# Performance work log

Hardware: AMD Instinct MI355X
Metric: run time of the kernel (lower is better)

Reference implementation:

```python
import jax, jax.numpy as jnp
import numpy as np

B, S, H = 2, 2048, 1024
E, I, K = 8, 4096, 2


def setup_inputs() -> dict:
    key = jax.random.key(0)
    ks = jax.random.split(key, 5)
    scale_h = 1.0 / np.sqrt(H)
    scale_i = 1.0 / np.sqrt(I)
    x = jax.random.normal(ks[0], (B, S, H), dtype=jnp.float32)
    gate_w = jax.random.normal(ks[1], (E, H), dtype=jnp.float32) * scale_h   # router Linear weight [out=E, in=H]
    wg = jax.random.normal(ks[2], (E, I, H), dtype=jnp.float32) * scale_h    # gate_proj weights, stacked over experts
    wu = jax.random.normal(ks[3], (E, I, H), dtype=jnp.float32) * scale_h    # up_proj weights
    wd = jax.random.normal(ks[4], (E, H, I), dtype=jnp.float32) * scale_i    # down_proj weights
    return {"x": x, "gate_w": gate_w, "wg": wg, "wu": wu, "wd": wd}


def _moe_forward(x, gate_w, wg, wu, wd):
    b, s, h = x.shape
    x_flat = x.reshape(-1, h)                       # [T, H]
    logits = x_flat @ gate_w.T                      # [T, E]
    top_v, top_i = jax.lax.top_k(logits, K)         # [T, K]
    probs = jax.nn.softmax(top_v.astype(jnp.float32), axis=-1).astype(logits.dtype)  # [T, K]
    # per-token combine weight for each expert: sum_k probs[:,k] * 1[top_i[:,k]==e]
    one_hot = jax.nn.one_hot(top_i, E, dtype=probs.dtype)   # [T, K, E]
    combine = jnp.einsum('tk,tke->et', probs, one_hot)       # [E, T]
    # loop over experts via scan: acc += w_e * SwiGLU_e(x)
    def body(acc, ws):
        wge, wue, wde, we = ws
        hidden = jax.nn.silu(x_flat @ wge.T) * (x_flat @ wue.T)  # [T, I]
        return acc + we[:, None] * (hidden @ wde.T), None
    out, _ = jax.lax.scan(body, jnp.zeros_like(x_flat), (wg, wu, wd, combine))
    return out.reshape(b, s, h)


def reference(x, gate_w, wg, wu, wd):
    return _moe_forward(x, gate_w, wg, wu, wd)
```

## Files before the change

kernel.cpp:

```cpp
#include <hip/hip_runtime.h>
#include <math.h>

#define T_TOK 4096
#define H_DIM 1024
#define E_NUM 8
#define I_DIM 4096
#define KSPLIT 4

typedef __attribute__((ext_vector_type(4))) float f32x4;
typedef __attribute__((ext_vector_type(8))) short bf16x8;

__device__ inline unsigned short f2bf(float f) {
  unsigned int u = __float_as_uint(f);
  u += 0x7fffu + ((u >> 16) & 1u);
  return (unsigned short)(u >> 16);
}

__device__ inline void cvt_store4(unsigned short* dst, const float* src) {
  f32x4 v = *reinterpret_cast<const f32x4*>(src);
  ushort4 o;
  o.x = f2bf(v[0]); o.y = f2bf(v[1]); o.z = f2bf(v[2]); o.w = f2bf(v[3]);
  *reinterpret_cast<ushort4*>(dst) = o;
}

__device__ inline void gll16(const void* g, void* l) {
  __builtin_amdgcn_global_load_lds(
      (const __attribute__((address_space(1))) void*)g,
      (__attribute__((address_space(3))) void*)l, 16, 0, 0);
}

__global__ __launch_bounds__(64) void k_router(const float* __restrict__ x,
                                               const float* __restrict__ gw,
                                               unsigned short* __restrict__ xb,
                                               int2* __restrict__ tokE,
                                               float2* __restrict__ tokP,
                                               int* __restrict__ counts) {
  const int t = blockIdx.x;
  const int l = threadIdx.x;
  const float* xr = x + (size_t)t * H_DIM;
  unsigned short* xbr = xb ? xb + (size_t)t * H_DIM : nullptr;
  float acc[E_NUM];
#pragma unroll
  for (int e = 0; e < E_NUM; e++) acc[e] = 0.f;
  for (int h = l; h < H_DIM; h += 64) {
    float xv = xr[h];
    if (xbr) xbr[h] = f2bf(xv);
#pragma unroll
    for (int e = 0; e < E_NUM; e++) acc[e] += xv * gw[e * H_DIM + h];
  }
#pragma unroll
  for (int e = 0; e < E_NUM; e++) {
#pragma unroll
    for (int off = 32; off > 0; off >>= 1) acc[e] += __shfl_xor(acc[e], off);
  }
  if (l == 0) {
    float v0 = -1e30f, v1 = -1e30f;
    int e0 = 0, e1 = 0;
#pragma unroll
    for (int e = 0; e < E_NUM; e++) {
      float v = acc[e];
      if (v > v0) { v1 = v0; e1 = e0; v0 = v; e0 = e; }
      else if (v > v1) { v1 = v; e1 = e; }
    }
    float ex = expf(v1 - v0);
    float p0 = 1.f / (1.f + ex);
    float p1 = ex * p0;
    tokE[t] = make_int2(e0, e1);
    tokP[t] = make_float2(p0, p1);
    atomicAdd(&counts[e0], 1);
    atomicAdd(&counts[e1], 1);
  }
}

__global__ void k_offsets(const int* __restrict__ counts, int* __restrict__ offsets) {
  if (threadIdx.x == 0 && blockIdx.x == 0) {
    int s = 0;
    for (int e = 0; e < E_NUM; e++) { offsets[e] = s; s += counts[e]; }
    offsets[E_NUM] = s;
  }
}

__global__ __launch_bounds__(256) void k_scatter(const int2* __restrict__ tokE,
                                                 const float2* __restrict__ tokP,
                                                 const int* __restrict__ offsets,
                                                 int* __restrict__ cursor,
                                                 int* __restrict__ slot_tok,
                                                 float* __restrict__ slot_w) {
  int t = blockIdx.x * 256 + threadIdx.x;
  if (t >= T_TOK) return;
  int2 e = tokE[t];
  float2 p = tokP[t];
  int pos0 = atomicAdd(&cursor[e.x], 1);
  slot_tok[offsets[e.x] + pos0] = t;
  slot_w[offsets[e.x] + pos0] = p.x;
  int pos1 = atomicAdd(&cursor[e.y], 1);
  slot_tok[offsets[e.y] + pos1] = t;
  slot_w[offsets[e.y] + pos1] = p.y;
}

__global__ __launch_bounds__(256) void k_cvt(const float* __restrict__ src,
                                             unsigned short* __restrict__ dst,
                                             int n4) {
  int i = blockIdx.x * 256 + threadIdx.x;
  const int stride = gridDim.x * 256;
  for (; i < n4; i += stride) {
    f32x4 v = reinterpret_cast<const f32x4*>(src)[i];
    ushort4 o;
    o.x = f2bf(v[0]); o.y = f2bf(v[1]); o.z = f2bf(v[2]); o.w = f2bf(v[3]);
    reinterpret_cast<ushort4*>(dst)[i] = o;
  }
}

__global__ __launch_bounds__(256, 2) void k_gateup2(
    const unsigned short* __restrict__ xb, const unsigned short* __restrict__ wgb,
    const unsigned short* __restrict__ wub, const int* __restrict__ counts,
    const int* __restrict__ offsets, const int* __restrict__ slot_tok,
    unsigned short* __restrict__ hidden) {
  const int e = blockIdx.z;
  const int cnt = counts[e];
  const int m0 = blockIdx.y * 128;
  if (m0 >= cnt) return;
  const int n0 = blockIdx.x * 128;
  const int base = offsets[e];

  __shared__ unsigned short As[128 * 64];
  __shared__ unsigned short Bg[128 * 64];
  __shared__ unsigned short Bu[128 * 64];

  const int tid = threadIdx.x;
  const int wave = tid >> 6;
  const int lane = tid & 63;
  const int wm = (wave >> 1) * 64;
  const int wn = (wave & 1) * 64;
  const int lr = lane & 15;
  const int lk = lane >> 4;

  const int sr = lane >> 3;
  const int sc = lane & 7;
  const int swz = ((sc ^ sr) << 3);

  const size_t wbase = (size_t)e * I_DIM * H_DIM;
  const unsigned short* srcA[4];
  const unsigned short* srcBg[4];
  const unsigned short* srcBu[4];
  unsigned short* dstA[4];
  unsigned short* dstBg[4];
  unsigned short* dstBu[4];
#pragma unroll
  for (int i = 0; i < 4; i++) {
    int row = wave * 32 + i * 8 + sr;
    int gr = m0 + row; if (gr > cnt - 1) gr = cnt - 1;
    srcA[i]  = xb + (size_t)slot_tok[base + gr] * H_DIM + swz;
    srcBg[i] = wgb + wbase + (size_t)(n0 + row) * H_DIM + swz;
    srcBu[i] = wub + wbase + (size_t)(n0 + row) * H_DIM + swz;
    dstA[i]  = &As[(wave * 32 + i * 8) * 64];
    dstBg[i] = &Bg[(wave * 32 + i * 8) * 64];
    dstBu[i] = &Bu[(wave * 32 + i * 8) * 64];
  }

  f32x4 accg[4][4], accu[4][4];
#pragma unroll
  for (int i = 0; i < 4; i++)
#pragma unroll
    for (int j = 0; j < 4; j++) {
      accg[i][j] = (f32x4){0.f, 0.f, 0.f, 0.f};
      accu[i][j] = (f32x4){0.f, 0.f, 0.f, 0.f};
    }

  const int xorr = ((lr & 7) << 3);

  for (int k0 = 0; k0 < H_DIM; k0 += 64) {
#pragma unroll
    for (int i = 0; i < 4; i++) {
      gll16(srcA[i] + k0, dstA[i]);
      gll16(srcBg[i] + k0, dstBg[i]);
      gll16(srcBu[i] + k0, dstBu[i]);
    }
    __syncthreads();
#pragma unroll
    for (int kh = 0; kh < 2; kh++) {
      const int koff = (((kh * 4 + lk) << 3) ^ xorr);
      bf16x8 af[4];
#pragma unroll
      for (int mf = 0; mf < 4; mf++)
        af[mf] = *reinterpret_cast<const bf16x8*>(&As[(wm + mf * 16 + lr) * 64 + koff]);
#pragma unroll
      for (int nf = 0; nf < 4; nf++) {
        const int roff = (wn + nf * 16 + lr) * 64 + koff;
        bf16x8 bg = *reinterpret_cast<const bf16x8*>(&Bg[roff]);
        bf16x8 bu = *reinterpret_cast<const bf16x8*>(&Bu[roff]);
#pragma unroll
        for (int mf = 0; mf < 4; mf++) {
          accg[mf][nf] = __builtin_amdgcn_mfma_f32_16x16x32_bf16(af[mf], bg, accg[mf][nf], 0, 0, 0);
          accu[mf][nf] = __builtin_amdgcn_mfma_f32_16x16x32_bf16(af[mf], bu, accu[mf][nf], 0, 0, 0);
        }
      }
    }
    __syncthreads();
  }

#pragma unroll
  for (int mf = 0; mf < 4; mf++) {
#pragma unroll
    for (int j = 0; j < 4; j++) {
      int row = wm + mf * 16 + lk * 4 + j;
      if (m0 + row < cnt) {
        size_t hbase = (size_t)(base + m0 + row) * I_DIM;
#pragma unroll
        for (int nf = 0; nf < 4; nf++) {
          int col = n0 + wn + nf * 16 + lr;
          float g = accg[mf][nf][j];
          float u = accu[mf][nf][j];
          float h = g / (1.f + expf(-g)) * u;
          hidden[hbase + col] = f2bf(h);
        }
      }
    }
  }
}

__global__ __launch_bounds__(256, 2) void k_down6(
    const unsigned short* __restrict__ hidden, const unsigned short* __restrict__ wdb,
    const int* __restrict__ counts, const int* __restrict__ offsets,
    const int* __restrict__ slot_tok, const float* __restrict__ slot_w,
    float* __restrict__ out) {
  const int zz = blockIdx.z;
  const int e = zz >> 2;
  const int ks = zz & 3;
  const int cnt = counts[e];
  const int m0 = blockIdx.y * 128;
  if (m0 >= cnt) return;
  const int n0 = blockIdx.x * 128;
  const int base = offsets[e];
  const int kbeg = ks * (I_DIM / KSPLIT);
  const int kend = kbeg + I_DIM / KSPLIT;

  __shared__ unsigned short As[128 * 64];
  __shared__ unsigned short Bs[128 * 64];

  const int tid = threadIdx.x;
  const int wave = tid >> 6;
  const int lane = tid & 63;
  const int wm = (wave >> 1) * 64;
  const int wn = (wave & 1) * 64;
  const int lr = lane & 15;
  const int lk = lane >> 4;

  const int sr = lane >> 3;
  const int sc = lane & 7;
  const int swz = ((sc ^ sr) << 3);

  const unsigned short* srcA[4];
  const unsigned short* srcB[4];
  unsigned short* dstA[4];
  unsigned short* dstB[4];
#pragma unroll
  for (int i = 0; i < 4; i++) {
    int row = wave * 32 + i * 8 + sr;
    int gr = m0 + row; if (gr > cnt - 1) gr = cnt - 1;
    srcA[i] = hidden + (size_t)(base + gr) * I_DIM + swz;
    srcB[i] = wdb + (size_t)e * H_DIM * I_DIM + (size_t)(n0 + row) * I_DIM + swz;
    dstA[i] = &As[(wave * 32 + i * 8) * 64];
    dstB[i] = &Bs[(wave * 32 + i * 8) * 64];
  }

  f32x4 acc[4][4];
#pragma unroll
  for (int i = 0; i < 4; i++)
#pragma unroll
    for (int j = 0; j < 4; j++) acc[i][j] = (f32x4){0.f, 0.f, 0.f, 0.f};

  const int xorr = ((lr & 7) << 3);

  for (int k0 = kbeg; k0 < kend; k0 += 64) {
#pragma unroll
    for (int i = 0; i < 4; i++) {
      gll16(srcA[i] + k0, dstA[i]);
      gll16(srcB[i] + k0, dstB[i]);
    }
    __syncthreads();
#pragma unroll
    for (int kh = 0; kh < 2; kh++) {
      const int koff = (((kh * 4 + lk) << 3) ^ xorr);
      bf16x8 af[4];
#pragma unroll
      for (int mf = 0; mf < 4; mf++)
        af[mf] = *reinterpret_cast<const bf16x8*>(&As[(wm + mf * 16 + lr) * 64 + koff]);
#pragma unroll
      for (int nf = 0; nf < 4; nf++) {
        bf16x8 bf = *reinterpret_cast<const bf16x8*>(&Bs[(wn + nf * 16 + lr) * 64 + koff]);
#pragma unroll
        for (int mf = 0; mf < 4; mf++)
          acc[mf][nf] = __builtin_amdgcn_mfma_f32_16x16x32_bf16(af[mf], bf, acc[mf][nf], 0, 0, 0);
      }
    }
    __syncthreads();
  }

#pragma unroll
  for (int mf = 0; mf < 4; mf++) {
#pragma unroll
    for (int j = 0; j < 4; j++) {
      int row = wm + mf * 16 + lk * 4 + j;
      if (m0 + row < cnt) {
        int slot = base + m0 + row;
        int t = slot_tok[slot];
        float w = slot_w[slot];
#pragma unroll
        for (int nf = 0; nf < 4; nf++) {
          int col = n0 + wn + nf * 16 + lr;
          atomicAdd(&out[(size_t)t * H_DIM + col], w * acc[mf][nf][j]);
        }
      }
    }
  }
}

__global__ __launch_bounds__(256) void k_gateup_v1(
    const float* __restrict__ x, const float* __restrict__ wg,
    const float* __restrict__ wu, const int* __restrict__ counts,
    const int* __restrict__ offsets, const int* __restrict__ slot_tok,
    unsigned short* __restrict__ hidden) {
  const int e = blockIdx.z;
  const int cnt = counts[e];
  const int m0 = blockIdx.y * 128;
  if (m0 >= cnt) return;
  const int n0 = blockIdx.x * 128;
  const int base = offsets[e];

  __shared__ unsigned short As[128 * 40];
  __shared__ unsigned short Bgs[128 * 40];
  __shared__ unsigned short Bus[128 * 40];

  const int tid = threadIdx.x;
  const int wave = tid >> 6;
  const int lane = tid & 63;
  const int wm = (wave >> 1) * 64;
  const int wn = (wave & 1) * 64;
  const int lr = lane & 15;
  const int lk = lane >> 4;
  const int r_sub = tid >> 3;
  const int kq = (tid & 7) * 4;

  const float* wge = wg + (size_t)e * I_DIM * H_DIM;
  const float* wue = wu + (size_t)e * I_DIM * H_DIM;

  const float* aptr[4];
  const float* bgptr[4];
  const float* buptr[4];
#pragma unroll
  for (int p = 0; p < 4; p++) {
    int row = p * 32 + r_sub;
    int gr = m0 + row;
    if (gr > cnt - 1) gr = cnt - 1;
    aptr[p] = x + (size_t)slot_tok[base + gr] * H_DIM + kq;
    bgptr[p] = wge + (size_t)(n0 + row) * H_DIM + kq;
    buptr[p] = wue + (size_t)(n0 + row) * H_DIM + kq;
  }

  f32x4 accg[4][4], accu[4][4];
#pragma unroll
  for (int i = 0; i < 4; i++)
#pragma unroll
    for (int j = 0; j < 4; j++) {
      accg[i][j] = (f32x4){0.f, 0.f, 0.f, 0.f};
      accu[i][j] = (f32x4){0.f, 0.f, 0.f, 0.f};
    }

  for (int k0 = 0; k0 < H_DIM; k0 += 32) {
#pragma unroll
    for (int p = 0; p < 4; p++) {
      int row = p * 32 + r_sub;
      cvt_store4(&As[row * 40 + kq], aptr[p] + k0);
      cvt_store4(&Bgs[row * 40 + kq], bgptr[p] + k0);
      cvt_store4(&Bus[row * 40 + kq], buptr[p] + k0);
    }
    __syncthreads();
    bf16x8 af[4];
#pragma unroll
    for (int mf = 0; mf < 4; mf++)
      af[mf] = *reinterpret_cast<const bf16x8*>(&As[(wm + mf * 16 + lr) * 40 + lk * 8]);
#pragma unroll
    for (int nf = 0; nf < 4; nf++) {
      bf16x8 bg = *reinterpret_cast<const bf16x8*>(&Bgs[(wn + nf * 16 + lr) * 40 + lk * 8]);
      bf16x8 bu = *reinterpret_cast<const bf16x8*>(&Bus[(wn + nf * 16 + lr) * 40 + lk * 8]);
#pragma unroll
      for (int mf = 0; mf < 4; mf++) {
        accg[mf][nf] = __builtin_amdgcn_mfma_f32_16x16x32_bf16(af[mf], bg, accg[mf][nf], 0, 0, 0);
        accu[mf][nf] = __builtin_amdgcn_mfma_f32_16x16x32_bf16(af[mf], bu, accu[mf][nf], 0, 0, 0);
      }
    }
    __syncthreads();
  }

#pragma unroll
  for (int mf = 0; mf < 4; mf++) {
#pragma unroll
    for (int j = 0; j < 4; j++) {
      int row = wm + mf * 16 + lk * 4 + j;
      if (m0 + row < cnt) {
        size_t hbase = (size_t)(base + m0 + row) * I_DIM;
#pragma unroll
        for (int nf = 0; nf < 4; nf++) {
          int col = n0 + wn + nf * 16 + lr;
          float g = accg[mf][nf][j];
          float u = accu[mf][nf][j];
          float h = g / (1.f + expf(-g)) * u;
          hidden[hbase + col] = f2bf(h);
        }
      }
    }
  }
}

__global__ __launch_bounds__(256) void k_down_v1(
    const unsigned short* __restrict__ hidden, const float* __restrict__ wd,
    const int* __restrict__ counts, const int* __restrict__ offsets,
    const int* __restrict__ slot_tok, const float* __restrict__ slot_w,
    float* __restrict__ out) {
  const int e = blockIdx.z;
  const int cnt = counts[e];
  const int m0 = blockIdx.y * 128;
  if (m0 >= cnt) return;
  const int n0 = blockIdx.x * 128;
  const int base = offsets[e];

  __shared__ unsigned short As[128 * 40];
  __shared__ unsigned short Bs[128 * 40];

  const int tid = threadIdx.x;
  const int wave = tid >> 6;
  const int lane = tid & 63;
  const int wm = (wave >> 1) * 64;
  const int wn = (wave & 1) * 64;
  const int lr = lane & 15;
  const int lk = lane >> 4;
  const int r_sub = tid >> 3;
  const int kq = (tid & 7) * 4;

  const unsigned short* ap[4];
  const float* bp[4];
#pragma unroll
  for (int p = 0; p < 4; p++) {
    int row = p * 32 + r_sub;
    int gr = m0 + row;
    if (gr > cnt - 1) gr = cnt - 1;
    ap[p] = hidden + (size_t)(base + gr) * I_DIM + kq;
    bp[p] = wd + (size_t)e * H_DIM * I_DIM + (size_t)(n0 + row) * I_DIM + kq;
  }

  f32x4 acc[4][4];
#pragma unroll
  for (int i = 0; i < 4; i++)
#pragma unroll
    for (int j = 0; j < 4; j++) acc[i][j] = (f32x4){0.f, 0.f, 0.f, 0.f};

  for (int k0 = 0; k0 < I_DIM; k0 += 32) {
#pragma unroll
    for (int p = 0; p < 4; p++) {
      int row = p * 32 + r_sub;
      *reinterpret_cast<ushort4*>(&As[row * 40 + kq]) =
          *reinterpret_cast<const ushort4*>(ap[p] + k0);
      cvt_store4(&Bs[row * 40 + kq], bp[p] + k0);
    }
    __syncthreads();
    bf16x8 af[4];
#pragma unroll
    for (int mf = 0; mf < 4; mf++)
      af[mf] = *reinterpret_cast<const bf16x8*>(&As[(wm + mf * 16 + lr) * 40 + lk * 8]);
#pragma unroll
    for (int nf = 0; nf < 4; nf++) {
      bf16x8 bf = *reinterpret_cast<const bf16x8*>(&Bs[(wn + nf * 16 + lr) * 40 + lk * 8]);
#pragma unroll
      for (int mf = 0; mf < 4; mf++)
        acc[mf][nf] = __builtin_amdgcn_mfma_f32_16x16x32_bf16(af[mf], bf, acc[mf][nf], 0, 0, 0);
    }
    __syncthreads();
  }

#pragma unroll
  for (int mf = 0; mf < 4; mf++) {
#pragma unroll
    for (int j = 0; j < 4; j++) {
      int row = wm + mf * 16 + lk * 4 + j;
      if (m0 + row < cnt) {
        int slot = base + m0 + row;
        int t = slot_tok[slot];
        float w = slot_w[slot];
#pragma unroll
        for (int nf = 0; nf < 4; nf++) {
          int col = n0 + wn + nf * 16 + lr;
          atomicAdd(&out[(size_t)t * H_DIM + col], w * acc[mf][nf][j]);
        }
      }
    }
  }
}

extern "C" void kernel_launch(void* const* d_in, const int* in_sizes, int n_in,
                              void* d_out, int out_size, void* d_ws, size_t ws_size,
                              hipStream_t stream) {
  const float* x = (const float*)d_in[0];
  const float* gate_w = (const float*)d_in[1];
  const float* wg = (const float*)d_in[2];
  const float* wu = (const float*)d_in[3];
  const float* wd = (const float*)d_in[4];
  float* out = (float*)d_out;

  char* ws = (char*)d_ws;
  int* counts = (int*)(ws + 0);
  int* cursor = (int*)(ws + 64);
  int* offsets = (int*)(ws + 128);
  int2* tokE = (int2*)(ws + 256);
  float2* tokP = (float2*)(ws + 256 + 32768);
  int* slot_tok = (int*)(ws + 256 + 65536);
  float* slot_w = (float*)(ws + 256 + 98304);

  const size_t OFF_XB  = 262144;
  const size_t OFF_HID = OFF_XB + 8388608;
  const size_t OFF_WG  = OFF_HID + 67108864;
  const size_t OFF_WU  = OFF_WG + 67108864;
  const size_t NEED    = OFF_WU + 67108864;

  const bool fast = (ws_size >= NEED);
  unsigned short* xb = fast ? (unsigned short*)(ws + OFF_XB) : nullptr;

  hipMemsetAsync(d_ws, 0, 256, stream);
  hipMemsetAsync(d_out, 0, (size_t)T_TOK * H_DIM * sizeof(float), stream);

  k_router<<<T_TOK, 64, 0, stream>>>(x, gate_w, xb, tokE, tokP, counts);
  k_offsets<<<1, 64, 0, stream>>>(counts, offsets);
  k_scatter<<<T_TOK / 256, 256, 0, stream>>>(tokE, tokP, offsets, cursor, slot_tok, slot_w);

  if (fast) {
    unsigned short* hid = (unsigned short*)(ws + OFF_HID);
    unsigned short* wgb = (unsigned short*)(ws + OFF_WG);
    unsigned short* wub = (unsigned short*)(ws + OFF_WU);
    unsigned short* wdb = wgb;

    k_cvt<<<2048, 256, 0, stream>>>(wg, wgb, E_NUM * I_DIM * H_DIM / 4);
    k_cvt<<<2048, 256, 0, stream>>>(wu, wub, E_NUM * I_DIM * H_DIM / 4);
    k_gateup2<<<dim3(I_DIM / 128, 32, E_NUM), 256, 0, stream>>>(
        xb, wgb, wub, counts, offsets, slot_tok, hid);
    k_cvt<<<2048, 256, 0, stream>>>(wd, wdb, E_NUM * H_DIM * I_DIM / 4);
    k_down6<<<dim3(H_DIM / 128, 32, E_NUM * KSPLIT), 256, 0, stream>>>(
        hid, wdb, counts, offsets, slot_tok, slot_w, out);
  } else {
    unsigned short* hid = (unsigned short*)(ws + 131328);
    k_gateup_v1<<<dim3(I_DIM / 128, 32, E_NUM), 256, 0, stream>>>(
        x, wg, wu, counts, offsets, slot_tok, hid);
    k_down_v1<<<dim3(H_DIM / 128, 32, E_NUM), 256, 0, stream>>>(
        hid, wd, counts, offsets, slot_tok, slot_w, out);
  }
}
```

Before: 597.7 us.

## Replace atomic down-proj reduction with per-slot partials and gather, drop K-split

The down projection no longer splits K four ways and atomically adds into the output. Each slot's weighted row is written to a partial buffer that reuses the dead up-weight workspace, and a gather kernel then sums each token's two expert rows. The gate and up weight conversions are merged into one launch, the offsets kernel and output memset are removed, and expert offsets are computed inline. This removes atomic contention and launches, at the cost of fewer down-proj blocks and an extra pass over the partial buffer.

```diff
diff --git a/kernel.cpp b/kernel.cpp
--- a/kernel.cpp
+++ b/kernel.cpp
@@ -5,7 +5,6 @@
 #define H_DIM 1024
 #define E_NUM 8
 #define I_DIM 4096
-#define KSPLIT 4
 
 typedef __attribute__((ext_vector_type(4))) float f32x4;
 typedef __attribute__((ext_vector_type(8))) short bf16x8;
@@ -82,20 +81,29 @@
 
 __global__ __launch_bounds__(256) void k_scatter(const int2* __restrict__ tokE,
                                                  const float2* __restrict__ tokP,
-                                                 const int* __restrict__ offsets,
+                                                 const int* __restrict__ counts,
                                                  int* __restrict__ cursor,
                                                  int* __restrict__ slot_tok,
-                                                 float* __restrict__ slot_w) {
+                                                 float* __restrict__ slot_w,
+                                                 int* __restrict__ inv_slot) {
   int t = blockIdx.x * 256 + threadIdx.x;
   if (t >= T_TOK) return;
+  int offs[E_NUM];
+  int s = 0;
+#pragma unroll
+  for (int e = 0; e < E_NUM; e++) { offs[e] = s; s += counts[e]; }
   int2 e = tokE[t];
   float2 p = tokP[t];
   int pos0 = atomicAdd(&cursor[e.x], 1);
-  slot_tok[offsets[e.x] + pos0] = t;
-  slot_w[offsets[e.x] + pos0] = p.x;
+  int s0 = offs[e.x] + pos0;
+  slot_tok[s0] = t;
+  slot_w[s0] = p.x;
+  inv_slot[2 * t] = s0;
   int pos1 = atomicAdd(&cursor[e.y], 1);
-  slot_tok[offsets[e.y] + pos1] = t;
-  slot_w[offsets[e.y] + pos1] = p.y;
+  int s1 = offs[e.y] + pos1;
+  slot_tok[s1] = t;
+  slot_w[s1] = p.y;
+  inv_slot[2 * t + 1] = s1;
 }
 
 __global__ __launch_bounds__(256) void k_cvt(const float* __restrict__ src,
@@ -111,17 +119,40 @@
   }
 }
 
+__global__ __launch_bounds__(256) void k_cvt2(const float* __restrict__ srcA,
+                                              unsigned short* __restrict__ dstA,
+                                              const float* __restrict__ srcB,
+                                              unsigned short* __restrict__ dstB,
+                                              int n4) {
+  int i = blockIdx.x * 256 + threadIdx.x;
+  const int stride = gridDim.x * 256;
+  for (; i < 2 * n4; i += stride) {
+    const float* s = (i < n4) ? srcA : srcB;
+    unsigned short* d = (i < n4) ? dstA : dstB;
+    int j = (i < n4) ? i : i - n4;
+    f32x4 v = reinterpret_cast<const f32x4*>(s)[j];
+    ushort4 o;
+    o.x = f2bf(v[0]); o.y = f2bf(v[1]); o.z = f2bf(v[2]); o.w = f2bf(v[3]);
+    reinterpret_cast<ushort4*>(d)[j] = o;
+  }
+}
+
+__device__ inline int expert_base(const int* counts, int e) {
+  int s = 0;
+  for (int i = 0; i < e; i++) s += counts[i];
+  return s;
+}
+
 __global__ __launch_bounds__(256, 2) void k_gateup2(
     const unsigned short* __restrict__ xb, const unsigned short* __restrict__ wgb,
     const unsigned short* __restrict__ wub, const int* __restrict__ counts,
-    const int* __restrict__ offsets, const int* __restrict__ slot_tok,
-    unsigned short* __restrict__ hidden) {
+    const int* __restrict__ slot_tok, unsigned short* __restrict__ hidden) {
   const int e = blockIdx.z;
   const int cnt = counts[e];
   const int m0 = blockIdx.y * 128;
   if (m0 >= cnt) return;
   const int n0 = blockIdx.x * 128;
-  const int base = offsets[e];
+  const int base = expert_base(counts, e);
 
   __shared__ unsigned short As[128 * 64];
   __shared__ unsigned short Bg[128 * 64];
@@ -219,21 +250,16 @@
   }
 }
 
-__global__ __launch_bounds__(256, 2) void k_down6(
+__global__ __launch_bounds__(256, 2) void k_down7(
     const unsigned short* __restrict__ hidden, const unsigned short* __restrict__ wdb,
-    const int* __restrict__ counts, const int* __restrict__ offsets,
-    const int* __restrict__ slot_tok, const float* __restrict__ slot_w,
-    float* __restrict__ out) {
-  const int zz = blockIdx.z;
-  const int e = zz >> 2;
-  const int ks = zz & 3;
+    const int* __restrict__ counts, const int* __restrict__ slot_tok,
+    const float* __restrict__ slot_w, float* __restrict__ part) {
+  const int e = blockIdx.z;
   const int cnt = counts[e];
   const int m0 = blockIdx.y * 128;
   if (m0 >= cnt) return;
   const int n0 = blockIdx.x * 128;
-  const int base = offsets[e];
-  const int kbeg = ks * (I_DIM / KSPLIT);
-  const int kend = kbeg + I_DIM / KSPLIT;
+  const int base = expert_base(counts, e);
 
   __shared__ unsigned short As[128 * 64];
   __shared__ unsigned short Bs[128 * 64];
@@ -272,7 +298,7 @@
 
   const int xorr = ((lr & 7) << 3);
 
-  for (int k0 = kbeg; k0 < kend; k0 += 64) {
+  for (int k0 = 0; k0 < I_DIM; k0 += 64) {
 #pragma unroll
     for (int i = 0; i < 4; i++) {
       gll16(srcA[i] + k0, dstA[i]);
@@ -304,16 +330,32 @@
       int row = wm + mf * 16 + lk * 4 + j;
       if (m0 + row < cnt) {
         int slot = base + m0 + row;
-        int t = slot_tok[slot];
         float w = slot_w[slot];
+        float* prow = part + (size_t)slot * H_DIM;
 #pragma unroll
         for (int nf = 0; nf < 4; nf++) {
           int col = n0 + wn + nf * 16 + lr;
-          atomicAdd(&out[(size_t)t * H_DIM + col], w * acc[mf][nf][j]);
+          prow[col] = w * acc[mf][nf][j];
         }
       }
     }
   }
+}
+
+__global__ __launch_bounds__(256) void k_gather(const float* __restrict__ part,
+                                                const int* __restrict__ inv_slot,
+                                                float* __restrict__ out) {
+  int i = blockIdx.x * 256 + threadIdx.x;
+  const int n4 = T_TOK * H_DIM / 4;
+  if (i >= n4) return;
+  const int perrow = H_DIM / 4;
+  int t = i / perrow;
+  int c = i - t * perrow;
+  int s0 = inv_slot[2 * t];
+  int s1 = inv_slot[2 * t + 1];
+  f32x4 a = reinterpret_cast<const f32x4*>(part)[(size_t)s0 * perrow + c];
+  f32x4 b = reinterpret_cast<const f32x4*>(part)[(size_t)s1 * perrow + c];
+  reinterpret_cast<f32x4*>(out)[i] = a + b;
 }
 
 __global__ __launch_bounds__(256) void k_gateup_v1(
@@ -515,6 +557,7 @@
   float2* tokP = (float2*)(ws + 256 + 32768);
   int* slot_tok = (int*)(ws + 256 + 65536);
   float* slot_w = (float*)(ws + 256 + 98304);
+  int* inv_slot = (int*)(ws + 256 + 131072);
 
   const size_t OFF_XB  = 262144;
   const size_t OFF_HID = OFF_XB + 8388608;
@@ -526,27 +569,29 @@
   unsigned short* xb = fast ? (unsigned short*)(ws + OFF_XB) : nullptr;
 
   hipMemsetAsync(d_ws, 0, 256, stream);
-  hipMemsetAsync(d_out, 0, (size_t)T_TOK * H_DIM * sizeof(float), stream);
 
   k_router<<<T_TOK, 64, 0, stream>>>(x, gate_w, xb, tokE, tokP, counts);
-  k_offsets<<<1, 64, 0, stream>>>(counts, offsets);
-  k_scatter<<<T_TOK / 256, 256, 0, stream>>>(tokE, tokP, offsets, cursor, slot_tok, slot_w);
+  k_scatter<<<T_TOK / 256, 256, 0, stream>>>(tokE, tokP, counts, cursor,
+                                             slot_tok, slot_w, inv_slot);
 
   if (fast) {
     unsigned short* hid = (unsigned short*)(ws + OFF_HID);
     unsigned short* wgb = (unsigned short*)(ws + OFF_WG);
     unsigned short* wub = (unsigned short*)(ws + OFF_WU);
     unsigned short* wdb = wgb;
-
-    k_cvt<<<2048, 256, 0, stream>>>(wg, wgb, E_NUM * I_DIM * H_DIM / 4);
-    k_cvt<<<2048, 256, 0, stream>>>(wu, wub, E_NUM * I_DIM * H_DIM / 4);
+    float* part = (float*)(ws + OFF_WU);
+
+    k_cvt2<<<4096, 256, 0, stream>>>(wg, wgb, wu, wub, E_NUM * I_DIM * H_DIM / 4);
     k_gateup2<<<dim3(I_DIM / 128, 32, E_NUM), 256, 0, stream>>>(
-        xb, wgb, wub, counts, offsets, slot_tok, hid);
+        xb, wgb, wub, counts, slot_tok, hid);
     k_cvt<<<2048, 256, 0, stream>>>(wd, wdb, E_NUM * H_DIM * I_DIM / 4);
-    k_down6<<<dim3(H_DIM / 128, 32, E_NUM * KSPLIT), 256, 0, stream>>>(
-        hid, wdb, counts, offsets, slot_tok, slot_w, out);
+    k_down7<<<dim3(H_DIM / 128, 32, E_NUM), 256, 0, stream>>>(
+        hid, wdb, counts, slot_tok, slot_w, part);
+    k_gather<<<T_TOK * H_DIM / 4 / 256, 256, 0, stream>>>(part, inv_slot, out);
   } else {
-    unsigned short* hid = (unsigned short*)(ws + 131328);
+    unsigned short* hid = (unsigned short*)(ws + 131328 + 32768);
+    hipMemsetAsync(d_out, 0, (size_t)T_TOK * H_DIM * sizeof(float), stream);
+    k_offsets<<<1, 64, 0, stream>>>(counts, offsets);
     k_gateup_v1<<<dim3(I_DIM / 128, 32, E_NUM), 256, 0, stream>>>(
         x, wg, wu, counts, offsets, slot_tok, hid);
     k_down_v1<<<dim3(H_DIM / 128, 32, E_NUM), 256, 0, stream>>>(
```

Result: faster. 566.3 us (-5.3%).
